# Kernel tuning notes

Hardware: AMD Instinct MI355X
Metric: run time of the kernel (lower is better)

Reference implementation:

```python
import jax, jax.numpy as jnp
import numpy as np

N = 1024      # layer_size (power of 2)
B = 16384     # batch
DEPTH = 2     # Butterfly depth (default)


def _abcd_offsets(n):
    """Factor sizes n, n/2, ..., 2 and their offsets into the packed ABCD buffer.
    A factor of size m has ABCD of shape (2, 2, m//2, 2) = 2m complex pairs."""
    offs = []
    off = 0
    m = n
    while m >= 2:
        offs.append((m, off))
        off += 2 * m
        m //= 2
    return offs, off  # off == 4n - 4


def setup_inputs() -> dict:
    key = jax.random.key(0)
    k1, k2, k3 = jax.random.split(key, 3)
    _, total = _abcd_offsets(N)
    x = jax.random.normal(k1, (B, N), jnp.float32)
    perm_logit = jax.random.normal(k2, (DEPTH, 3), jnp.float32)
    # scale ~1/sqrt(2) so the product of log2(n) random 2x2 blocks stays bounded
    abcd = jax.random.normal(k3, (DEPTH, total, 2), jnp.float32) * 0.7
    b = jnp.zeros((N,), jnp.float32)
    return {"x": x, "perm_logit": perm_logit, "abcd": abcd, "b": b}


def _perm_factor(h, p, m):
    """One BlockPerm factor (soft permutation) of size m applied blockwise.
    h: (B, n, 2) real/imag pairs. p: (3,) probabilities.
    p[0]: mix with even/odd separation; p[1], p[2]: mix each half with its reversal."""
    Bn, n, _ = h.shape
    h = h.reshape(Bn, n // m, m, 2)
    eo = jnp.concatenate([h[:, :, 0::2], h[:, :, 1::2]], axis=2)
    h = (1 - p[0]) * h + p[0] * eo
    h1, h2 = h[:, :, : m // 2], h[:, :, m // 2 :]
    h1 = (1 - p[1]) * h1 + p[1] * h1[:, :, ::-1]
    h2 = (1 - p[2]) * h2 + p[2] * h2[:, :, ::-1]
    return jnp.concatenate([h1, h2], axis=2).reshape(Bn, n, 2)


def _diag_factor(h, ABCD, m):
    """One Block2x2Diag factor of size m: out = [[A,B],[C,D]] x with diagonal A,B,C,D.
    h: (B, n, 2); ABCD: (2, 2, m//2, 2) complex pairs."""
    Bn, n, _ = h.shape
    hv = h.reshape(Bn, n // m, 2, m // 2, 2)  # (B, blocks, halves, m/2, cplx)
    xr, xi = hv[..., 0], hv[..., 1]
    Ar, Ai = ABCD[..., 0], ABCD[..., 1]
    yr = jnp.einsum('ijk,bnjk->bnik', Ar, xr) - jnp.einsum('ijk,bnjk->bnik', Ai, xi)
    yi = jnp.einsum('ijk,bnjk->bnik', Ar, xi) + jnp.einsum('ijk,bnjk->bnik', Ai, xr)
    return jnp.stack([yr, yi], axis=-1).reshape(Bn, n, 2)


def _forward(x, perm_logit, abcd, b):
    n = x.shape[-1]
    offs, _ = _abcd_offsets(n)
    # real_to_complex: (B, n) -> (B, n, 2)
    h = jnp.stack([x, jnp.zeros_like(x)], axis=-1)
    perm_sizes = [m for (m, _) in offs if m >= 4]
    depth = perm_logit.shape[0]
    for d in range(depth):
        # BlockPermProduct (share_logit=True): all factors share one (3,) logit
        p = jax.nn.sigmoid(perm_logit[d])
        for m in reversed(perm_sizes):      # smallest factor first
            h = _perm_factor(h, p, m)
        # Block2x2DiagProduct: factors applied smallest size first
        for (m, off) in reversed(offs):
            ABCD = abcd[d, off:off + 2 * m].reshape(2, 2, m // 2, 2)
            h = _diag_factor(h, ABCD, m)
    out = h[..., 0]  # take real part
    return b + out


def reference(x, perm_logit, abcd, b):
    return _forward(x, perm_logit, abcd, b)
```

## Files before the change

kernel.cpp:

```cpp
#include <hip/hip_runtime.h>
#include <hip/hip_bf16.h>
#include <stdint.h>

#define N_DIM 1024
#define DEPTH 2
#define ABCD_TOTAL 4092

typedef __attribute__((ext_vector_type(8))) short short8;
typedef __attribute__((ext_vector_type(4))) float floatx4;

__global__ __launch_bounds__(256) void build_and_cast(
    const float* __restrict__ perm_logit,
    const float* __restrict__ abcd,
    const float* __restrict__ x,
    __hip_bfloat16* __restrict__ S,
    __hip_bfloat16* __restrict__ xb)
{
    const int bx  = blockIdx.x;
    const int tid = threadIdx.x;
    __shared__ float2 h[2][2][N_DIM];

    if (bx >= 512) {
        const int cb = bx - 512;
        const size_t i = ((size_t)cb * 256 + tid) * 8;
        float4 v0 = *(const float4*)(x + i);
        float4 v1 = *(const float4*)(x + i + 4);
        union { __hip_bfloat16 e[8]; int4 v; } u;
        u.e[0] = __float2bfloat16(v0.x); u.e[1] = __float2bfloat16(v0.y);
        u.e[2] = __float2bfloat16(v0.z); u.e[3] = __float2bfloat16(v0.w);
        u.e[4] = __float2bfloat16(v1.x); u.e[5] = __float2bfloat16(v1.y);
        u.e[6] = __float2bfloat16(v1.z); u.e[7] = __float2bfloat16(v1.w);
        *(int4*)(xb + i) = u.v;
        return;
    }

    const int row0 = bx * 2;
    const float2 zz = make_float2(0.0f, 0.0f);
    for (int j = tid; j < N_DIM; j += 256) {
        h[0][0][j] = zz; h[0][1][j] = zz;
        h[1][0][j] = zz; h[1][1][j] = zz;
    }
    __syncthreads();
    if (tid < 2) h[tid][0][row0 + tid] = make_float2(1.0f, 0.0f);
    __syncthreads();

    int cur = 0;
    for (int d = 0; d < DEPTH; ++d) {
        const float p0 = 1.0f / (1.0f + expf(-perm_logit[d * 3 + 0]));
        const float p1 = 1.0f / (1.0f + expf(-perm_logit[d * 3 + 1]));
        const float p2 = 1.0f / (1.0f + expf(-perm_logit[d * 3 + 2]));

        for (int s = 2; s <= 10; ++s) {
            const int half = 1 << (s - 1), hq = half >> 1;
            const int cnt   = (d == 0) ? half : 512;
            const int pbase = (d == 0) ? ((row0 >> s) << (s - 1)) : 0;
            for (int vt = tid; vt < 2 * cnt; vt += 256) {
                const int v = (vt < cnt) ? 0 : 1;
                const int t = pbase + (v ? vt - cnt : vt);
                const float2* __restrict__ in  = h[v][cur];
                float2* __restrict__ out       = h[v][cur ^ 1];
                const int blk  = t >> (s - 1);
                const int r    = t & (half - 1);
                const int base = blk << s;
                int q1, q2; float pc;
                if (r < hq) { q1 = r;           q2 = half - 1 - r;   pc = p1; }
                else        { int r2 = r - hq;  q1 = half + r2;
                              q2 = 2 * half - 1 - r2;                pc = p2; }
                const int src1 = (q1 < half) ? 2 * q1 : 2 * (q1 - half) + 1;
                const int src2 = (q2 < half) ? 2 * q2 : 2 * (q2 - half) + 1;
                float2 b1 = in[base + q1], a1 = in[base + src1];
                float2 b2 = in[base + q2], a2 = in[base + src2];
                float2 s1a, s1b, o1, o2;
                s1a.x = b1.x + p0 * (a1.x - b1.x);  s1a.y = b1.y + p0 * (a1.y - b1.y);
                s1b.x = b2.x + p0 * (a2.x - b2.x);  s1b.y = b2.y + p0 * (a2.y - b2.y);
                o1.x = s1a.x + pc * (s1b.x - s1a.x); o1.y = s1a.y + pc * (s1b.y - s1a.y);
                o2.x = s1b.x + pc * (s1a.x - s1b.x); o2.y = s1b.y + pc * (s1a.y - s1b.y);
                out[base + q1] = o1;
                out[base + q2] = o2;
            }
            __syncthreads();
            cur ^= 1;
        }

        for (int s = 1; s <= 10; ++s) {
            const int m = 1 << s, half = m >> 1;
            const int off = 4096 - 4 * m;
            const float* __restrict__ ab = abcd + (size_t)d * (ABCD_TOTAL * 2) + (size_t)off * 2;
            for (int vt = tid; vt < 1024; vt += 256) {
                const int v = vt >> 9;
                const int t = vt & 511;
                const float2* __restrict__ in = h[v][cur];
                float2* __restrict__ out      = h[v][cur ^ 1];
                const int blk  = t >> (s - 1);
                const int k    = t & (half - 1);
                const int base = blk << s;
                float2 xt = in[base + k];
                float2 xb2 = in[base + half + k];
                float2 A  = *(const float2*)(ab + 2 * (size_t)k);
                float2 Bc = *(const float2*)(ab + 2 * (size_t)(half + k));
                float2 Cc = *(const float2*)(ab + 2 * (size_t)(m + k));
                float2 Dc = *(const float2*)(ab + 2 * (size_t)(m + half + k));
                float2 yt, yb;
                yt.x = A.x * xt.x - A.y * xt.y + Bc.x * xb2.x - Bc.y * xb2.y;
                yt.y = A.x * xt.y + A.y * xt.x + Bc.x * xb2.y + Bc.y * xb2.x;
                yb.x = Cc.x * xt.x - Cc.y * xt.y + Dc.x * xb2.x - Dc.y * xb2.y;
                yb.y = Cc.x * xt.y + Cc.y * xt.x + Dc.x * xb2.y + Dc.y * xb2.x;
                out[base + k]        = yt;
                out[base + half + k] = yb;
            }
            __syncthreads();
            cur ^= 1;
        }
    }

    for (int j = tid; j < N_DIM; j += 256) {
        S[(size_t)row0 * N_DIM + j]       = __float2bfloat16(h[0][cur][j].x);
        S[(size_t)(row0 + 1) * N_DIM + j] = __float2bfloat16(h[1][cur][j].x);
    }
}

__global__ __launch_bounds__(256) void transpose_w(
    const __hip_bfloat16* __restrict__ S, __hip_bfloat16* __restrict__ Wt)
{
    const int i0 = (blockIdx.x & 15) * 64;
    const int j0 = (blockIdx.x >> 4) * 64;
    __shared__ __hip_bfloat16 tile[64][72];
    const int r  = threadIdx.x >> 2;
    const int c0 = (threadIdx.x & 3) * 16;
    *(short8*)&tile[r][c0]     = *(const short8*)(S + (size_t)(i0 + r) * N_DIM + j0 + c0);
    *(short8*)&tile[r][c0 + 8] = *(const short8*)(S + (size_t)(i0 + r) * N_DIM + j0 + c0 + 8);
    __syncthreads();
    union { __hip_bfloat16 e[8]; short8 v; } o1, o2;
#pragma unroll
    for (int k = 0; k < 8; ++k) { o1.e[k] = tile[c0 + k][r]; o2.e[k] = tile[c0 + 8 + k][r]; }
    *(short8*)(Wt + (size_t)(j0 + r) * N_DIM + i0 + c0)     = o1.v;
    *(short8*)(Wt + (size_t)(j0 + r) * N_DIM + i0 + c0 + 8) = o2.v;
}

#define BM 128
#define BN 128
#define BK 32

__device__ __forceinline__ void gl_lds16(const void* g, void* l) {
    __builtin_amdgcn_global_load_lds(
        (const __attribute__((address_space(1))) uint32_t*)g,
        (__attribute__((address_space(3))) uint32_t*)l, 16, 0, 0);
}

__global__ __launch_bounds__(256) void gemm_bt(
    const __hip_bfloat16* __restrict__ A,
    const __hip_bfloat16* __restrict__ Bt,
    const float* __restrict__ bias,
    float* __restrict__ C)
{
    const int tid = threadIdx.x;
    const int bx  = blockIdx.x;
    const int xcd = bx & 7;
    const int loc = bx >> 3;
    const int m0  = (xcd * 16 + (loc >> 3)) * BM;
    const int n0  = (loc & 7) * BN;

    __shared__ __hip_bfloat16 sA[BM * BK];
    __shared__ __hip_bfloat16 sB[BN * BK];

    const int lane = tid & 63;
    const int wm   = ((tid >> 6) & 1) * 64;
    const int wn   = ((tid >> 6) >> 1) * 64;
    const int lrow = lane & 15;
    const int lq   = lane >> 4;

    const int r1  = tid >> 2;
    const int c1s = (tid & 3) ^ ((tid >> 3) & 3);
    const int swz = (lrow >> 1) & 3;
    const int ca  = lq ^ swz;

    floatx4 acc[4][4] = {};

    for (int kt = 0; kt < 32; ++kt) {
        const int k0 = kt * BK;
        gl_lds16(A  + (size_t)(m0 + r1)      * N_DIM + k0 + c1s * 8, (char*)sA + tid * 16);
        gl_lds16(A  + (size_t)(m0 + 64 + r1) * N_DIM + k0 + c1s * 8, (char*)sA + (tid + 256) * 16);
        gl_lds16(Bt + (size_t)(n0 + r1)      * N_DIM + k0 + c1s * 8, (char*)sB + tid * 16);
        gl_lds16(Bt + (size_t)(n0 + 64 + r1) * N_DIM + k0 + c1s * 8, (char*)sB + (tid + 256) * 16);
        __syncthreads();

        short8 af[4], bf[4];
#pragma unroll
        for (int i = 0; i < 4; ++i) {
            af[i] = *(const short8*)((const char*)sA + ((wm + i * 16 + lrow) * 4 + ca) * 16);
            bf[i] = *(const short8*)((const char*)sB + ((wn + i * 16 + lrow) * 4 + ca) * 16);
        }
#pragma unroll
        for (int i = 0; i < 4; ++i)
#pragma unroll
            for (int j = 0; j < 4; ++j)
                acc[i][j] = __builtin_amdgcn_mfma_f32_16x16x32_bf16(
                    af[i], bf[j], acc[i][j], 0, 0, 0);
        __syncthreads();
    }

#pragma unroll
    for (int j = 0; j < 4; ++j) {
        const int gn = n0 + wn + j * 16 + lrow;
        const float bv = bias[gn];
#pragma unroll
        for (int i = 0; i < 4; ++i) {
            const int gm = m0 + wm + i * 16 + lq * 4;
#pragma unroll
            for (int r = 0; r < 4; ++r)
                C[(size_t)(gm + r) * N_DIM + gn] = acc[i][j][r] + bv;
        }
    }
}

extern "C" void kernel_launch(void* const* d_in, const int* in_sizes, int n_in,
                              void* d_out, int out_size, void* d_ws, size_t ws_size,
                              hipStream_t stream) {
    const float* x          = (const float*)d_in[0];
    const float* perm_logit = (const float*)d_in[1];
    const float* abcd       = (const float*)d_in[2];
    const float* bias       = (const float*)d_in[3];
    float* out              = (float*)d_out;

    __hip_bfloat16* S  = (__hip_bfloat16*)d_out;
    __hip_bfloat16* Wt = (__hip_bfloat16*)d_ws;
    __hip_bfloat16* xb = (__hip_bfloat16*)((char*)d_ws + (1 << 21));

    build_and_cast<<<dim3(512 + 8192), dim3(256), 0, stream>>>(perm_logit, abcd, x, S, xb);
    transpose_w<<<dim3(256), dim3(256), 0, stream>>>(S, Wt);
    gemm_bt<<<dim3(1024), dim3(256), 0, stream>>>(xb, Wt, bias, out);
}
```

Measured before the change: 189.2 us.

## Pack two rows per float4 and fuse butterfly diag stages in pairs

The matrix-building kernel now stores both basis rows it handles interleaved in one float4 per position, so each thread moves two rows' complex values per shared-memory access. Pairs of consecutive Block2x2Diag factors are fused into one radix-4 style pass, halving the number of barriers and shared-memory round trips for those stages. The shared buffer shrinks and loops are unrolled. This only affects the small W-construction prologue; the main GEMM is untouched, so the overall effect depends on how much of the time that prologue takes.

```diff
diff --git a/kernel.cpp b/kernel.cpp
--- a/kernel.cpp
+++ b/kernel.cpp
@@ -8,6 +8,16 @@
 
 typedef __attribute__((ext_vector_type(8))) short short8;
 typedef __attribute__((ext_vector_type(4))) float floatx4;
+typedef __attribute__((ext_vector_type(4))) float f4;
+
+__device__ __forceinline__ f4 cmul(float cr, float ci, f4 v) {
+    f4 r;
+    r[0] = cr * v[0] - ci * v[1];
+    r[1] = cr * v[1] + ci * v[0];
+    r[2] = cr * v[2] - ci * v[3];
+    r[3] = cr * v[3] + ci * v[2];
+    return r;
+}
 
 __global__ __launch_bounds__(256) void build_and_cast(
     const float* __restrict__ perm_logit,
@@ -18,7 +28,7 @@
 {
     const int bx  = blockIdx.x;
     const int tid = threadIdx.x;
-    __shared__ float2 h[2][2][N_DIM];
+    __shared__ f4 h[2][N_DIM];
 
     if (bx >= 512) {
         const int cb = bx - 512;
@@ -35,13 +45,15 @@
     }
 
     const int row0 = bx * 2;
-    const float2 zz = make_float2(0.0f, 0.0f);
-    for (int j = tid; j < N_DIM; j += 256) {
-        h[0][0][j] = zz; h[0][1][j] = zz;
-        h[1][0][j] = zz; h[1][1][j] = zz;
-    }
+    const f4 zz = {0.0f, 0.0f, 0.0f, 0.0f};
+    for (int j = tid; j < N_DIM; j += 256) { h[0][j] = zz; h[1][j] = zz; }
     __syncthreads();
-    if (tid < 2) h[tid][0][row0 + tid] = make_float2(1.0f, 0.0f);
+    if (tid == 0) {
+        f4 e0 = {1.0f, 0.0f, 0.0f, 0.0f};
+        f4 e1 = {0.0f, 0.0f, 1.0f, 0.0f};
+        h[0][row0]     = e0;
+        h[0][row0 + 1] = e1;
+    }
     __syncthreads();
 
     int cur = 0;
@@ -50,15 +62,15 @@
         const float p1 = 1.0f / (1.0f + expf(-perm_logit[d * 3 + 1]));
         const float p2 = 1.0f / (1.0f + expf(-perm_logit[d * 3 + 2]));
 
+#pragma unroll
         for (int s = 2; s <= 10; ++s) {
             const int half = 1 << (s - 1), hq = half >> 1;
             const int cnt   = (d == 0) ? half : 512;
             const int pbase = (d == 0) ? ((row0 >> s) << (s - 1)) : 0;
-            for (int vt = tid; vt < 2 * cnt; vt += 256) {
-                const int v = (vt < cnt) ? 0 : 1;
-                const int t = pbase + (v ? vt - cnt : vt);
-                const float2* __restrict__ in  = h[v][cur];
-                float2* __restrict__ out       = h[v][cur ^ 1];
+            const f4* __restrict__ in = h[cur];
+            f4* __restrict__ out      = h[cur ^ 1];
+            for (int tt = tid; tt < cnt; tt += 256) {
+                const int t    = pbase + tt;
                 const int blk  = t >> (s - 1);
                 const int r    = t & (half - 1);
                 const int base = blk << s;
@@ -68,45 +80,53 @@
                               q2 = 2 * half - 1 - r2;                pc = p2; }
                 const int src1 = (q1 < half) ? 2 * q1 : 2 * (q1 - half) + 1;
                 const int src2 = (q2 < half) ? 2 * q2 : 2 * (q2 - half) + 1;
-                float2 b1 = in[base + q1], a1 = in[base + src1];
-                float2 b2 = in[base + q2], a2 = in[base + src2];
-                float2 s1a, s1b, o1, o2;
-                s1a.x = b1.x + p0 * (a1.x - b1.x);  s1a.y = b1.y + p0 * (a1.y - b1.y);
-                s1b.x = b2.x + p0 * (a2.x - b2.x);  s1b.y = b2.y + p0 * (a2.y - b2.y);
-                o1.x = s1a.x + pc * (s1b.x - s1a.x); o1.y = s1a.y + pc * (s1b.y - s1a.y);
-                o2.x = s1b.x + pc * (s1a.x - s1b.x); o2.y = s1b.y + pc * (s1a.y - s1b.y);
-                out[base + q1] = o1;
-                out[base + q2] = o2;
+                f4 b1 = in[base + q1], a1 = in[base + src1];
+                f4 b2 = in[base + q2], a2 = in[base + src2];
+                f4 s1a = b1 + p0 * (a1 - b1);
+                f4 s1b = b2 + p0 * (a2 - b2);
+                out[base + q1] = s1a + pc * (s1b - s1a);
+                out[base + q2] = s1b + pc * (s1a - s1b);
             }
             __syncthreads();
             cur ^= 1;
         }
 
-        for (int s = 1; s <= 10; ++s) {
-            const int m = 1 << s, half = m >> 1;
-            const int off = 4096 - 4 * m;
-            const float* __restrict__ ab = abcd + (size_t)d * (ABCD_TOTAL * 2) + (size_t)off * 2;
-            for (int vt = tid; vt < 1024; vt += 256) {
-                const int v = vt >> 9;
-                const int t = vt & 511;
-                const float2* __restrict__ in = h[v][cur];
-                float2* __restrict__ out      = h[v][cur ^ 1];
-                const int blk  = t >> (s - 1);
-                const int k    = t & (half - 1);
-                const int base = blk << s;
-                float2 xt = in[base + k];
-                float2 xb2 = in[base + half + k];
-                float2 A  = *(const float2*)(ab + 2 * (size_t)k);
-                float2 Bc = *(const float2*)(ab + 2 * (size_t)(half + k));
-                float2 Cc = *(const float2*)(ab + 2 * (size_t)(m + k));
-                float2 Dc = *(const float2*)(ab + 2 * (size_t)(m + half + k));
-                float2 yt, yb;
-                yt.x = A.x * xt.x - A.y * xt.y + Bc.x * xb2.x - Bc.y * xb2.y;
-                yt.y = A.x * xt.y + A.y * xt.x + Bc.x * xb2.y + Bc.y * xb2.x;
-                yb.x = Cc.x * xt.x - Cc.y * xt.y + Dc.x * xb2.x - Dc.y * xb2.y;
-                yb.y = Cc.x * xt.y + Cc.y * xt.x + Dc.x * xb2.y + Dc.y * xb2.x;
-                out[base + k]        = yt;
-                out[base + half + k] = yb;
+        const float* __restrict__ abd = abcd + (size_t)d * (ABCD_TOTAL * 2);
+#pragma unroll
+        for (int s = 1; s <= 9; s += 2) {
+            const int hh = 1 << (s - 1);
+            const float* __restrict__ ab1 = abd + (size_t)(4096 - 8 * hh) * 2;
+            const float* __restrict__ ab2 = abd + (size_t)(4096 - 16 * hh) * 2;
+            const f4* __restrict__ in = h[cur];
+            f4* __restrict__ out      = h[cur ^ 1];
+            {
+                const int g     = tid;
+                const int k     = g & (hh - 1);
+                const int base2 = (g >> (s - 1)) << (s + 1);
+                f4 x0 = in[base2 + k];
+                f4 x1 = in[base2 + k + hh];
+                f4 x2 = in[base2 + k + 2 * hh];
+                f4 x3 = in[base2 + k + 3 * hh];
+                float2 A = *(const float2*)(ab1 + 2 * (size_t)k);
+                float2 B = *(const float2*)(ab1 + 2 * (size_t)(hh + k));
+                float2 C = *(const float2*)(ab1 + 2 * (size_t)(2 * hh + k));
+                float2 D = *(const float2*)(ab1 + 2 * (size_t)(3 * hh + k));
+                f4 y0 = cmul(A.x, A.y, x0) + cmul(B.x, B.y, x1);
+                f4 y1 = cmul(C.x, C.y, x0) + cmul(D.x, D.y, x1);
+                f4 y2 = cmul(A.x, A.y, x2) + cmul(B.x, B.y, x3);
+                f4 y3 = cmul(C.x, C.y, x2) + cmul(D.x, D.y, x3);
+                float2 A2 = *(const float2*)(ab2 + 2 * (size_t)k);
+                float2 B2 = *(const float2*)(ab2 + 2 * (size_t)(2 * hh + k));
+                float2 C2 = *(const float2*)(ab2 + 2 * (size_t)(4 * hh + k));
+                float2 D2 = *(const float2*)(ab2 + 2 * (size_t)(6 * hh + k));
+                float2 A3 = *(const float2*)(ab2 + 2 * (size_t)(hh + k));
+                float2 B3 = *(const float2*)(ab2 + 2 * (size_t)(3 * hh + k));
+                float2 C3 = *(const float2*)(ab2 + 2 * (size_t)(5 * hh + k));
+                float2 D3 = *(const float2*)(ab2 + 2 * (size_t)(7 * hh + k));
+                out[base2 + k]          = cmul(A2.x, A2.y, y0) + cmul(B2.x, B2.y, y2);
+                out[base2 + k + 2 * hh] = cmul(C2.x, C2.y, y0) + cmul(D2.x, D2.y, y2);
+                out[base2 + k + hh]     = cmul(A3.x, A3.y, y1) + cmul(B3.x, B3.y, y3);
+                out[base2 + k + 3 * hh] = cmul(C3.x, C3.y, y1) + cmul(D3.x, D3.y, y3);
             }
             __syncthreads();
             cur ^= 1;
@@ -114,8 +134,9 @@
     }
 
     for (int j = tid; j < N_DIM; j += 256) {
-        S[(size_t)row0 * N_DIM + j]       = __float2bfloat16(h[0][cur][j].x);
-        S[(size_t)(row0 + 1) * N_DIM + j] = __float2bfloat16(h[1][cur][j].x);
+        f4 v = h[cur][j];
+        S[(size_t)row0 * N_DIM + j]       = __float2bfloat16(v[0]);
+        S[(size_t)(row0 + 1) * N_DIM + j] = __float2bfloat16(v[2]);
     }
 }
 
```

Measured after the change: 164.8 us. 1.15x faster.
